# Kernel tuning notes

Measured on AMD Instinct MI355X. Metric: run time of the kernel, lower is better.

## Reference

```python
import jax, jax.numpy as jnp
import numpy as np

RATES = (6, 12, 18, 24)  # dilation/padding per branch


def _offset_conv(x, w, b, rate):
    # mmcv ConvModule with norm_cfg=None: conv (bias=True) + ReLU
    y = jax.lax.conv_general_dilated(
        x, w, window_strides=(1, 1),
        padding=[(rate, rate), (rate, rate)],
        rhs_dilation=(rate, rate),
        dimension_numbers=('NCHW', 'OIHW', 'NCHW'))
    return jax.nn.relu(y + b[None, :, None, None])


def _deform_conv(x, offset, w, rate):
    # DCNv1: 3x3 deformable conv, stride 1, padding=dilation=rate,
    # deformable_groups=1, no bias. Zero padding outside image (bilinear).
    B, C, H, W = x.shape
    K = 9  # 3x3 kernel taps, row-major; offset channels [2k]=dy, [2k+1]=dx
    ky = (jnp.arange(K) // 3 - 1).astype(x.dtype)
    kx = (jnp.arange(K) % 3 - 1).astype(x.dtype)
    off = offset.reshape(B, K, 2, H, W)
    gy = jnp.arange(H, dtype=x.dtype)
    gx = jnp.arange(W, dtype=x.dtype)
    # sampling coords [B,K,H,W]: p0 + dilated kernel offset + learned offset
    py = gy[None, None, :, None] + ky[None, :, None, None] * rate + off[:, :, 0]
    px = gx[None, None, None, :] + kx[None, :, None, None] * rate + off[:, :, 1]
    y0 = jnp.floor(py)
    x0 = jnp.floor(px)
    wy = (py - y0)[:, None]  # [B,1,K,H,W]
    wx = (px - x0)[:, None]
    y0i = y0.astype(jnp.int32)
    x0i = x0.astype(jnp.int32)
    xf = x.reshape(B, C, H * W)

    def gather(yi, xi):
        valid = (yi >= 0) & (yi < H) & (xi >= 0) & (xi < W)
        idx = (jnp.clip(yi, 0, H - 1) * W + jnp.clip(xi, 0, W - 1)).reshape(B, K * H * W)
        v = jnp.take_along_axis(xf, idx[:, None, :], axis=2).reshape(B, C, K, H, W)
        return v * valid[:, None].astype(x.dtype)

    samp = (gather(y0i, x0i) * (1 - wy) * (1 - wx)
            + gather(y0i, x0i + 1) * (1 - wy) * wx
            + gather(y0i + 1, x0i) * wy * (1 - wx)
            + gather(y0i + 1, x0i + 1) * wy * wx)  # [B,C,K,H,W]
    return jnp.einsum('oik,bikhw->bohw', w.reshape(w.shape[0], C, K), samp)


def setup_inputs() -> dict:
    key = jax.random.key(0)
    k1, k2, k3 = jax.random.split(key, 3)
    B, C, H, W = 2, 256, 64, 64
    Cout, R = 256, len(RATES)
    x = jax.random.normal(k1, (B, C, H, W), dtype=jnp.float32)
    dweights = jax.random.normal(k2, (R, Cout, C, 3, 3), dtype=jnp.float32) * 0.02
    oweights = jax.random.normal(k3, (R, 18, C, 3, 3), dtype=jnp.float32) * 0.01
    obias = jnp.zeros((R, 18), dtype=jnp.float32)
    return {"x": x, "dweights": dweights, "oweights": oweights, "obias": obias}


def reference(x, dweights, oweights, obias):
    R = len(RATES)
    outs = []
    for i in range(R):
        j = (i - 1) % R  # source quirk: offsets[i-1] (wraps to last for i=0)
        off = _offset_conv(x, oweights[j], obias[j], RATES[j])
        outs.append(_deform_conv(x, off, dweights[i], RATES[i]))
    return jnp.concatenate(outs, axis=1)
```

## Files before the change

kernel.cpp:

```cpp
#include <hip/hip_runtime.h>
#include <hip/hip_bf16.h>

typedef __attribute__((ext_vector_type(4))) float f32x4;
typedef __attribute__((ext_vector_type(2))) _Float16 h2;
typedef __attribute__((ext_vector_type(8))) _Float16 f16x8;

#define LGKM_BARRIER() asm volatile("s_waitcnt lgkmcnt(0)\n\ts_barrier" ::: "memory")

__device__ __forceinline__ uint4 lerp4(uint4 c0, uint4 c1, uint4 c2, uint4 c3,
                                       h2 qx, h2 qy, h2 qz, h2 qv) {
    h2 r0 = (*(h2*)&c0.x) * qx + (*(h2*)&c1.x) * qy + (*(h2*)&c2.x) * qz + (*(h2*)&c3.x) * qv;
    h2 r1 = (*(h2*)&c0.y) * qx + (*(h2*)&c1.y) * qy + (*(h2*)&c2.y) * qz + (*(h2*)&c3.y) * qv;
    h2 r2 = (*(h2*)&c0.z) * qx + (*(h2*)&c1.z) * qy + (*(h2*)&c2.z) * qz + (*(h2*)&c3.z) * qv;
    h2 r3 = (*(h2*)&c0.w) * qx + (*(h2*)&c1.w) * qy + (*(h2*)&c2.w) * qz + (*(h2*)&c3.w) * qv;
    return make_uint4(*(unsigned*)&r0, *(unsigned*)&r1, *(unsigned*)&r2, *(unsigned*)&r3);
}

__global__ __launch_bounds__(256) void transpose_x_hwc_f16(const float* __restrict__ x,
                                                           unsigned short* __restrict__ x16h) {
    __shared__ float s[64][65];
    int blk = blockIdx.x;
    int b = blk >> 8, ct = (blk >> 6) & 3, pt = blk & 63;
    int c0 = ct * 64, p0 = pt * 64;
    int tid = threadIdx.x;
    int tr = tid >> 6, tc = tid & 63;
#pragma unroll
    for (int i = 0; i < 16; ++i) {
        int c = i * 4 + tr;
        s[c][tc] = x[((size_t)b * 256 + c0 + c) * 4096 + p0 + tc];
    }
    __syncthreads();
#pragma unroll
    for (int i = 0; i < 16; ++i) {
        int pp = i * 4 + tr;
        _Float16 h = (_Float16)s[tc][pp];
        x16h[((size_t)b * 4096 + p0 + pp) * 256 + c0 + tc] = *(unsigned short*)&h;
    }
}

__global__ __launch_bounds__(256) void transpose_dw_f16(const float* __restrict__ dw,
                                                        unsigned short* __restrict__ wTh) {
    __shared__ float s[2304];
    int blk = blockIdx.x;
    int i = blk >> 8, o = blk & 255;
    const float* src = dw + (size_t)(i * 256 + o) * 2304;
    int tid = threadIdx.x;
#pragma unroll
    for (int e = tid; e < 576; e += 256)
        *(float4*)&s[e * 4] = *(const float4*)&src[e * 4];
    __syncthreads();
#pragma unroll
    for (int k = 0; k < 9; ++k) {
        _Float16 h = (_Float16)s[tid * 9 + k];
        wTh[(((size_t)i * 9 + k) * 256 + o) * 256 + tid] = *(unsigned short*)&h;
    }
}

__global__ __launch_bounds__(256) void transpose_ow_f16(const float* __restrict__ ow,
                                                        unsigned short* __restrict__ owTh) {
    int idx = blockIdx.x * 256 + threadIdx.x;
    int c = idx & 255;
    int m = (idx >> 8) & 31;
    int rk = idx >> 13;
    int k = rk % 9, r = rk / 9;
    float v = (m < 18) ? ow[((r * 18 + m) * 256 + c) * 9 + k] : 0.f;
    _Float16 h = (_Float16)v;
    owTh[idx] = *(unsigned short*)&h;
}

__global__ __launch_bounds__(512) void offset_mfma3f(const unsigned short* __restrict__ x16h,
                                                     const unsigned short* __restrict__ owTh,
                                                     const float* __restrict__ obias,
                                                     float* __restrict__ off) {
    __shared__ short    s_a[8][32][8];
    __shared__ short    s_b[8][128][8];
    __shared__ int      s_pix[9][128];
    __shared__ unsigned s_msk[9][128];

    const int blk = blockIdx.x;
    const int r = (blk & 7) >> 1, b = blk & 1;
    const int px0 = (blk >> 3) << 7;
    const int rate = 6 * (r + 1);

    const int tid = threadIdx.x;
    const int lane = tid & 63;
    const int w = tid >> 6;
    const int kg = lane >> 4, lm = lane & 15;
    const int sg = tid >> 7, spx = tid & 127;
    const int mA = (tid & 127) >> 2, kgA = tid & 3;

    const unsigned short* xbh = x16h + (size_t)b * 1048576;
    const unsigned short* wrb = owTh + (size_t)r * 9 * 32 * 256;

    for (int e = tid; e < 1152; e += 512) {
        int k = e >> 7, pl = e & 127;
        int pg = px0 + pl;
        int yy = (pg >> 6) + (k / 3 - 1) * rate;
        int xx = (pg & 63) + (k % 3 - 1) * rate;
        bool v = ((unsigned)yy < 64u) && ((unsigned)xx < 64u);
        int cy = min(max(yy, 0), 63), cx = min(max(xx, 0), 63);
        s_pix[k][pl] = cy * 64 + cx;
        s_msk[k][pl] = v ? 0xFFFFFFFFu : 0u;
    }
    __syncthreads();

    f32x4 acc0 = (f32x4)(0.f), acc1 = (f32x4)(0.f);

    uint4 a_lo, a_hi, v_lo, v_hi;
    if (tid < 128) {
        a_lo = *(const uint4*)(wrb + (size_t)mA * 256 + kgA * 8);
        a_hi = *(const uint4*)(wrb + (size_t)mA * 256 + 32 + kgA * 8);
    }
    {
        int pix = s_pix[0][spx];
        v_lo = *(const uint4*)(xbh + (size_t)pix * 256 + sg * 8);
        v_hi = *(const uint4*)(xbh + (size_t)pix * 256 + 32 + sg * 8);
    }
    unsigned m = s_msk[0][spx];

    for (int t = 0; t < 36; ++t) {
        uint4 pkl = make_uint4(v_lo.x & m, v_lo.y & m, v_lo.z & m, v_lo.w & m);
        uint4 pkh = make_uint4(v_hi.x & m, v_hi.y & m, v_hi.z & m, v_hi.w & m);

        LGKM_BARRIER();
        if (tid < 128) {
            *(uint4*)&s_a[kgA][mA][0]     = a_lo;
            *(uint4*)&s_a[kgA + 4][mA][0] = a_hi;
        }
        *(uint4*)&s_b[sg][spx][0]     = pkl;
        *(uint4*)&s_b[sg + 4][spx][0] = pkh;
        LGKM_BARRIER();

        if (t < 35) {
            int tn = t + 1, tapn = tn >> 2, c0n = (tn & 3) << 6;
            if (tid < 128) {
                a_lo = *(const uint4*)(wrb + ((size_t)tapn * 32 + mA) * 256 + c0n + kgA * 8);
                a_hi = *(const uint4*)(wrb + ((size_t)tapn * 32 + mA) * 256 + c0n + 32 + kgA * 8);
            }
            int pix = s_pix[tapn][spx];
            m = s_msk[tapn][spx];
            v_lo = *(const uint4*)(xbh + (size_t)pix * 256 + c0n + sg * 8);
            v_hi = *(const uint4*)(xbh + (size_t)pix * 256 + c0n + 32 + sg * 8);
        }

#pragma unroll
        for (int kf = 0; kf < 2; ++kf) {
            int oct = kf * 4 + kg;
            f16x8 bf  = *(const f16x8*)&s_b[oct][w * 16 + lm][0];
            f16x8 af0 = *(const f16x8*)&s_a[oct][lm][0];
            f16x8 af1 = *(const f16x8*)&s_a[oct][16 + lm][0];
            acc0 = __builtin_amdgcn_mfma_f32_16x16x32_f16(af0, bf, acc0, 0, 0, 0);
            acc1 = __builtin_amdgcn_mfma_f32_16x16x32_f16(af1, bf, acc1, 0, 0, 0);
        }
    }

    const float* bias = obias + r * 18;
    float* ob = off + (size_t)(r * 2 + b) * 18 * 4096;
    int px = px0 + w * 16 + lm;
#pragma unroll
    for (int reg = 0; reg < 4; ++reg) {
        int mm = kg * 4 + reg;
        ob[(size_t)mm * 4096 + px] = fmaxf(acc0[reg] + bias[mm], 0.f);
        int m1 = 16 + mm;
        if (m1 < 18)
            ob[(size_t)m1 * 4096 + px] = fmaxf(acc1[reg] + bias[m1], 0.f);
    }
}

__global__ __launch_bounds__(512, 2) void deform_mfma14(const unsigned short* __restrict__ x16h,
                                                        const unsigned short* __restrict__ wTh,
                                                        const float* __restrict__ off,
                                                        float* __restrict__ out) {
    __shared__ short s_a[2][256][64];
    __shared__ short s_b[2][64][64];

    const int blk = blockIdx.x;
    const int i = (blk & 7) >> 1, b = blk & 1;
    const int px0 = (blk >> 3) << 6;
    const int r = (i + 3) & 3;
    const int rate = 6 * (i + 1);

    const int tid = threadIdx.x;
    const int lane = tid & 63;
    const int w = tid >> 6;
    const int wo = w >> 1, wp = w & 1;
    const int kg = lane >> 4, lm = lane & 15;
    const int pxS = tid >> 3, chgS = tid & 7;
    const int oA = tid >> 3, partA = tid & 7;
    const int colA = (partA ^ (oA & 7)) * 8;

    const unsigned short* xbh = x16h + (size_t)b * 1048576;
    const float* offb = off + (size_t)(r * 2 + b) * 18 * 4096;
    const unsigned short* wib = wTh + (size_t)i * 9 * 65536;

    const int pg = px0 + pxS;
    const int yy = pg >> 6, xc = pg & 63;

    auto coords = [&](int k, float dy, float dx, int4& P, float4& Q) {
        float py = (float)(yy + (k / 3 - 1) * rate) + dy;
        float pxf = (float)(xc + (k % 3 - 1) * rate) + dx;
        float fy = floorf(py), fx = floorf(pxf);
        int y0 = (int)fy, x0 = (int)fx;
        float wy = py - fy, wx = pxf - fx;
        float vy0 = ((unsigned)y0 < 64u) ? 1.f : 0.f;
        float vy1 = ((unsigned)(y0 + 1) < 64u) ? 1.f : 0.f;
        float vx0 = ((unsigned)x0 < 64u) ? 1.f : 0.f;
        float vx1 = ((unsigned)(x0 + 1) < 64u) ? 1.f : 0.f;
        int cy0 = min(max(y0, 0), 63), cy1 = min(max(y0 + 1, 0), 63);
        int cx0 = min(max(x0, 0), 63), cx1 = min(max(x0 + 1, 0), 63);
        P = make_int4(cy0 * 64 + cx0, cy0 * 64 + cx1, cy1 * 64 + cx0, cy1 * 64 + cx1);
        Q = make_float4(vy0 * vx0 * (1.f - wy) * (1.f - wx),
                        vy0 * vx1 * (1.f - wy) * wx,
                        vy1 * vx0 * wy * (1.f - wx),
                        vy1 * vx1 * wy * wx);
    };

    f32x4 acc[4][2];
#pragma unroll
    for (int mi = 0; mi < 4; ++mi) {
        acc[mi][0] = (f32x4)(0.f);
        acc[mi][1] = (f32x4)(0.f);
    }

    uint4 a0, a1, a2, a3, v0, v1, v2, v3;

    auto load_step = [&](int t, int4 P) {
        int tap = t >> 2, c0 = (t & 3) << 6;
        const unsigned short* wrow = wib + (size_t)tap * 65536 + c0 + partA * 8;
        a0 = *(const uint4*)(wrow + (size_t)(oA      ) * 256);
        a1 = *(const uint4*)(wrow + (size_t)(oA +  64) * 256);
        a2 = *(const uint4*)(wrow + (size_t)(oA + 128) * 256);
        a3 = *(const uint4*)(wrow + (size_t)(oA + 192) * 256);
        const unsigned short* xch = xbh + c0 + chgS * 8;
        v0 = *(const uint4*)(xch + ((size_t)P.x << 8));
        v1 = *(const uint4*)(xch + ((size_t)P.y << 8));
        v2 = *(const uint4*)(xch + ((size_t)P.z << 8));
        v3 = *(const uint4*)(xch + ((size_t)P.w << 8));
    };

    auto stage_step = [&](int buf, float4 Q) {
        h2 qx = (h2)((_Float16)Q.x), qy = (h2)((_Float16)Q.y);
        h2 qz = (h2)((_Float16)Q.z), qv = (h2)((_Float16)Q.w);
        uint4 pk = lerp4(v0, v1, v2, v3, qx, qy, qz, qv);
        *(uint4*)&s_a[buf][oA      ][colA] = a0;
        *(uint4*)&s_a[buf][oA +  64][colA] = a1;
        *(uint4*)&s_a[buf][oA + 128][colA] = a2;
        *(uint4*)&s_a[buf][oA + 192][colA] = a3;
        *(uint4*)&s_b[buf][pxS][(chgS ^ (pxS & 7)) * 8] = pk;
    };

    int4 P;  float4 Q;
    int4 Pn; float4 Qn;
    float dyn, dxn;
    {
        float dy0 = offb[pg];
        float dx0 = offb[4096 + pg];
        coords(0, dy0, dx0, P, Q);
    }
    load_step(0, P);
    stage_step(0, Q);
    load_step(1, P);
    LGKM_BARRIER();

    for (int tap = 0; tap < 9; ++tap) {
#pragma unroll
        for (int sub = 0; sub < 4; ++sub) {
            const int t = tap * 4 + sub;
            const int rb = t & 1;

            if (sub == 0 && tap < 8) {
                dyn = offb[(size_t)(2 * (tap + 1)) * 4096 + pg];
                dxn = offb[(size_t)(2 * (tap + 1) + 1) * 4096 + pg];
            }
            if (sub == 1 && tap < 8)
                coords(tap + 1, dyn, dxn, Pn, Qn);

            if (t < 35) stage_step(rb ^ 1, (sub == 3 && tap < 8) ? Qn : Q);
            if (t < 34) load_step(t + 2, (sub >= 2 && tap < 8) ? Pn : P);

#pragma unroll
            for (int kf = 0; kf < 2; ++kf) {
                int oct = kf * 4 + kg;
                int bcol = (oct ^ (lm & 7)) * 8;
                f16x8 bf0 = *(const f16x8*)&s_b[rb][wp * 32 + lm][bcol];
                f16x8 bf1 = *(const f16x8*)&s_b[rb][wp * 32 + 16 + lm][bcol];
#pragma unroll
                for (int mi = 0; mi < 4; ++mi) {
                    int o = wo * 64 + mi * 16 + lm;
                    int col = (oct ^ (o & 7)) * 8;
                    f16x8 af = *(const f16x8*)&s_a[rb][o][col];
                    acc[mi][0] = __builtin_amdgcn_mfma_f32_16x16x32_f16(af, bf0, acc[mi][0], 0, 0, 0);
                    acc[mi][1] = __builtin_amdgcn_mfma_f32_16x16x32_f16(af, bf1, acc[mi][1], 0, 0, 0);
                }
            }

            LGKM_BARRIER();

            if (sub == 3 && tap < 8) { P = Pn; Q = Qn; }
        }
    }

    float* ob = out + ((size_t)b * 1024 + i * 256) * 4096;
#pragma unroll
    for (int mi = 0; mi < 4; ++mi) {
        int o = wo * 64 + mi * 16 + kg * 4;
#pragma unroll
        for (int ni = 0; ni < 2; ++ni) {
            int pgo = px0 + wp * 32 + ni * 16 + lm;
#pragma unroll
            for (int reg = 0; reg < 4; ++reg)
                ob[(size_t)(o + reg) * 4096 + pgo] = acc[mi][ni][reg];
        }
    }
}

extern "C" void kernel_launch(void* const* d_in, const int* in_sizes, int n_in,
                              void* d_out, int out_size, void* d_ws, size_t ws_size,
                              hipStream_t stream) {
    const float* x  = (const float*)d_in[0];
    const float* dw = (const float*)d_in[1];
    const float* ow = (const float*)d_in[2];
    const float* ob = (const float*)d_in[3];
    float* out = (float*)d_out;

    float* ws  = (float*)d_ws;
    float* off = ws;
    unsigned short* wTh  = (unsigned short*)(ws + 589824);
    unsigned short* owTh = wTh + 2359296;
    unsigned short* x16h = (unsigned short*)(ws + 1916928);

    transpose_x_hwc_f16<<<512, 256, 0, stream>>>(x, x16h);
    transpose_dw_f16<<<1024, 256, 0, stream>>>(dw, wTh);
    transpose_ow_f16<<<1152, 256, 0, stream>>>(ow, owTh);
    offset_mfma3f<<<256, 512, 0, stream>>>(x16h, owTh, ob, off);
    deform_mfma14<<<512, 512, 0, stream>>>(x16h, wTh, off, out);
}
```

Measured before the change: 115.2 us.

## Preformat deform weights into MFMA fragment layout and load A operands from global to registers

```diff
diff --git a/kernel.cpp b/kernel.cpp
--- a/kernel.cpp
+++ b/kernel.cpp
@@ -38,8 +38,8 @@
     }
 }
 
-__global__ __launch_bounds__(256) void transpose_dw_f16(const float* __restrict__ dw,
-                                                        unsigned short* __restrict__ wTh) {
+__global__ __launch_bounds__(256) void transpose_dw_frag(const float* __restrict__ dw,
+                                                         unsigned short* __restrict__ wfrag) {
     __shared__ float s[2304];
     int blk = blockIdx.x;
     int i = blk >> 8, o = blk & 255;
@@ -49,10 +49,12 @@
     for (int e = tid; e < 576; e += 256)
         *(float4*)&s[e * 4] = *(const float4*)&src[e * 4];
     __syncthreads();
+    int oct = (tid >> 3) & 7, e = tid & 7, sub = tid >> 6;
 #pragma unroll
     for (int k = 0; k < 9; ++k) {
         _Float16 h = (_Float16)s[tid * 9 + k];
-        wTh[(((size_t)i * 9 + k) * 256 + o) * 256 + tid] = *(unsigned short*)&h;
+        int t = k * 4 + sub;
+        wfrag[(((size_t)i * 36 + t) * 8 + oct) * 2048 + o * 8 + e] = *(unsigned short*)&h;
     }
 }
 
@@ -167,11 +169,10 @@
     }
 }
 
-__global__ __launch_bounds__(512, 2) void deform_mfma14(const unsigned short* __restrict__ x16h,
-                                                        const unsigned short* __restrict__ wTh,
+__global__ __launch_bounds__(512, 2) void deform_mfma15(const unsigned short* __restrict__ x16h,
+                                                        const unsigned short* __restrict__ wfrag,
                                                         const float* __restrict__ off,
                                                         float* __restrict__ out) {
-    __shared__ short s_a[2][256][64];
     __shared__ short s_b[2][64][64];
 
     const int blk = blockIdx.x;
@@ -186,12 +187,12 @@
     const int wo = w >> 1, wp = w & 1;
     const int kg = lane >> 4, lm = lane & 15;
     const int pxS = tid >> 3, chgS = tid & 7;
-    const int oA = tid >> 3, partA = tid & 7;
-    const int colA = (partA ^ (oA & 7)) * 8;
 
     const unsigned short* xbh = x16h + (size_t)b * 1048576;
     const float* offb = off + (size_t)(r * 2 + b) * 18 * 4096;
-    const unsigned short* wib = wTh + (size_t)i * 9 * 65536;
+    const unsigned short* wfi = wfrag + (size_t)i * 36 * 16384;
+    const unsigned short* wlaneA = wfi + (size_t)(kg    ) * 2048 + (size_t)(wo * 64 + lm) * 8;
+    const unsigned short* wlaneB = wfi + (size_t)(kg + 4) * 2048 + (size_t)(wo * 64 + lm) * 8;
 
     const int pg = px0 + pxS;
     const int yy = pg >> 6, xc = pg & 63;
@@ -222,30 +223,33 @@
         acc[mi][1] = (f32x4)(0.f);
     }
 
-    uint4 a0, a1, a2, a3, v0, v1, v2, v3;
-
-    auto load_step = [&](int t, int4 P) {
-        int tap = t >> 2, c0 = (t & 3) << 6;
-        const unsigned short* wrow = wib + (size_t)tap * 65536 + c0 + partA * 8;
-        a0 = *(const uint4*)(wrow + (size_t)(oA      ) * 256);
-        a1 = *(const uint4*)(wrow + (size_t)(oA +  64) * 256);
-        a2 = *(const uint4*)(wrow + (size_t)(oA + 128) * 256);
-        a3 = *(const uint4*)(wrow + (size_t)(oA + 192) * 256);
+    uint4 aA0, aA1, aA2, aA3, aB0, aB1, aB2, aB3;
+    uint4 v0, v1, v2, v3;
+
+    auto load_corners = [&](int t, int4 P) {
+        int c0 = (t & 3) << 6;
         const unsigned short* xch = xbh + c0 + chgS * 8;
         v0 = *(const uint4*)(xch + ((size_t)P.x << 8));
         v1 = *(const uint4*)(xch + ((size_t)P.y << 8));
         v2 = *(const uint4*)(xch + ((size_t)P.z << 8));
         v3 = *(const uint4*)(xch + ((size_t)P.w << 8));
     };
-
-    auto stage_step = [&](int buf, float4 Q) {
+    auto load_A = [&](int t) {
+        const unsigned short* ba = wlaneA + (size_t)t * 16384;
+        aA0 = *(const uint4*)(ba);
+        aA1 = *(const uint4*)(ba + 128);
+        aA2 = *(const uint4*)(ba + 256);
+        aA3 = *(const uint4*)(ba + 384);
+        const unsigned short* bb = wlaneB + (size_t)t * 16384;
+        aB0 = *(const uint4*)(bb);
+        aB1 = *(const uint4*)(bb + 128);
+        aB2 = *(const uint4*)(bb + 256);
+        aB3 = *(const uint4*)(bb + 384);
+    };
+    auto stage_B = [&](int buf, float4 Q) {
         h2 qx = (h2)((_Float16)Q.x), qy = (h2)((_Float16)Q.y);
         h2 qz = (h2)((_Float16)Q.z), qv = (h2)((_Float16)Q.w);
         uint4 pk = lerp4(v0, v1, v2, v3, qx, qy, qz, qv);
-        *(uint4*)&s_a[buf][oA      ][colA] = a0;
-        *(uint4*)&s_a[buf][oA +  64][colA] = a1;
-        *(uint4*)&s_a[buf][oA + 128][colA] = a2;
-        *(uint4*)&s_a[buf][oA + 192][colA] = a3;
         *(uint4*)&s_b[buf][pxS][(chgS ^ (pxS & 7)) * 8] = pk;
     };
 
@@ -257,9 +261,10 @@
         float dx0 = offb[4096 + pg];
         coords(0, dy0, dx0, P, Q);
     }
-    load_step(0, P);
-    stage_step(0, Q);
-    load_step(1, P);
+    load_corners(0, P);
+    stage_B(0, Q);
+    load_corners(1, P);
+    load_A(0);
     LGKM_BARRIER();
 
     for (int tap = 0; tap < 9; ++tap) {
@@ -275,24 +280,35 @@
             if (sub == 1 && tap < 8)
                 coords(tap + 1, dyn, dxn, Pn, Qn);
 
-            if (t < 35) stage_step(rb ^ 1, (sub == 3 && tap < 8) ? Qn : Q);
-            if (t < 34) load_step(t + 2, (sub >= 2 && tap < 8) ? Pn : P);
-
-#pragma unroll
-            for (int kf = 0; kf < 2; ++kf) {
-                int oct = kf * 4 + kg;
-                int bcol = (oct ^ (lm & 7)) * 8;
-                f16x8 bf0 = *(const f16x8*)&s_b[rb][wp * 32 + lm][bcol];
-                f16x8 bf1 = *(const f16x8*)&s_b[rb][wp * 32 + 16 + lm][bcol];
-#pragma unroll
-                for (int mi = 0; mi < 4; ++mi) {
-                    int o = wo * 64 + mi * 16 + lm;
-                    int col = (oct ^ (o & 7)) * 8;
-                    f16x8 af = *(const f16x8*)&s_a[rb][o][col];
-                    acc[mi][0] = __builtin_amdgcn_mfma_f32_16x16x32_f16(af, bf0, acc[mi][0], 0, 0, 0);
-                    acc[mi][1] = __builtin_amdgcn_mfma_f32_16x16x32_f16(af, bf1, acc[mi][1], 0, 0, 0);
-                }
+            if (t < 35) stage_B(rb ^ 1, (sub == 3 && tap < 8) ? Qn : Q);
+            if (t < 34) load_corners(t + 2, (sub >= 2 && tap < 8) ? Pn : P);
+
+            {
+                int bc0 = (kg ^ (lm & 7)) * 8;
+                f16x8 b00 = *(const f16x8*)&s_b[rb][wp * 32 + lm][bc0];
+                f16x8 b01 = *(const f16x8*)&s_b[rb][wp * 32 + 16 + lm][bc0];
+                acc[0][0] = __builtin_amdgcn_mfma_f32_16x16x32_f16(*(const f16x8*)&aA0, b00, acc[0][0], 0, 0, 0);
+                acc[0][1] = __builtin_amdgcn_mfma_f32_16x16x32_f16(*(const f16x8*)&aA0, b01, acc[0][1], 0, 0, 0);
+                acc[1][0] = __builtin_amdgcn_mfma_f32_16x16x32_f16(*(const f16x8*)&aA1, b00, acc[1][0], 0, 0, 0);
+                acc[1][1] = __builtin_amdgcn_mfma_f32_16x16x32_f16(*(const f16x8*)&aA1, b01, acc[1][1], 0, 0, 0);
+                acc[2][0] = __builtin_amdgcn_mfma_f32_16x16x32_f16(*(const f16x8*)&aA2, b00, acc[2][0], 0, 0, 0);
+                acc[2][1] = __builtin_amdgcn_mfma_f32_16x16x32_f16(*(const f16x8*)&aA2, b01, acc[2][1], 0, 0, 0);
+                acc[3][0] = __builtin_amdgcn_mfma_f32_16x16x32_f16(*(const f16x8*)&aA3, b00, acc[3][0], 0, 0, 0);
+                acc[3][1] = __builtin_amdgcn_mfma_f32_16x16x32_f16(*(const f16x8*)&aA3, b01, acc[3][1], 0, 0, 0);
+                int bc1 = ((kg + 4) ^ (lm & 7)) * 8;
+                f16x8 b10 = *(const f16x8*)&s_b[rb][wp * 32 + lm][bc1];
+                f16x8 b11 = *(const f16x8*)&s_b[rb][wp * 32 + 16 + lm][bc1];
+                acc[0][0] = __builtin_amdgcn_mfma_f32_16x16x32_f16(*(const f16x8*)&aB0, b10, acc[0][0], 0, 0, 0);
+                acc[0][1] = __builtin_amdgcn_mfma_f32_16x16x32_f16(*(const f16x8*)&aB0, b11, acc[0][1], 0, 0, 0);
+                acc[1][0] = __builtin_amdgcn_mfma_f32_16x16x32_f16(*(const f16x8*)&aB1, b10, acc[1][0], 0, 0, 0);
+                acc[1][1] = __builtin_amdgcn_mfma_f32_16x16x32_f16(*(const f16x8*)&aB1, b11, acc[1][1], 0, 0, 0);
+                acc[2][0] = __builtin_amdgcn_mfma_f32_16x16x32_f16(*(const f16x8*)&aB2, b10, acc[2][0], 0, 0, 0);
+                acc[2][1] = __builtin_amdgcn_mfma_f32_16x16x32_f16(*(const f16x8*)&aB2, b11, acc[2][1], 0, 0, 0);
+                acc[3][0] = __builtin_amdgcn_mfma_f32_16x16x32_f16(*(const f16x8*)&aB3, b10, acc[3][0], 0, 0, 0);
+                acc[3][1] = __builtin_amdgcn_mfma_f32_16x16x32_f16(*(const f16x8*)&aB3, b11, acc[3][1], 0, 0, 0);
             }
+
+            if (t < 35) load_A(t + 1);
 
             LGKM_BARRIER();
 
@@ -325,13 +341,13 @@
 
     float* ws  = (float*)d_ws;
     float* off = ws;
-    unsigned short* wTh  = (unsigned short*)(ws + 589824);
-    unsigned short* owTh = wTh + 2359296;
-    unsigned short* x16h = (unsigned short*)(ws + 1916928);
+    unsigned short* wfrag = (unsigned short*)(ws + 589824);
+    unsigned short* owTh  = wfrag + 2359296;
+    unsigned short* x16h  = (unsigned short*)(ws + 1916928);
 
     transpose_x_hwc_f16<<<512, 256, 0, stream>>>(x, x16h);
-    transpose_dw_f16<<<1024, 256, 0, stream>>>(dw, wTh);
+    transpose_dw_frag<<<1024, 256, 0, stream>>>(dw, wfrag);
     transpose_ow_f16<<<1152, 256, 0, stream>>>(ow, owTh);
     offset_mfma3f<<<256, 512, 0, stream>>>(x16h, owTh, ob, off);
-    deform_mfma14<<<512, 512, 0, stream>>>(x16h, wTh, off, out);
-}
+    deform_mfma15<<<512, 512, 0, stream>>>(x16h, wfrag, off, out);
+}
```

Result: no change. 116.8 us (+1.4%).

## Split deform conv output channels across blocks and single-buffer LDS staging

Applied to the files above, without the earlier changes.

```diff
diff --git a/kernel.cpp b/kernel.cpp
--- a/kernel.cpp
+++ b/kernel.cpp
@@ -167,16 +167,18 @@
     }
 }
 
-__global__ __launch_bounds__(512, 2) void deform_mfma14(const unsigned short* __restrict__ x16h,
+__global__ __launch_bounds__(256, 4) void deform_mfma16(const unsigned short* __restrict__ x16h,
                                                         const unsigned short* __restrict__ wTh,
                                                         const float* __restrict__ off,
                                                         float* __restrict__ out) {
-    __shared__ short s_a[2][256][64];
-    __shared__ short s_b[2][64][64];
+    __shared__ short s_a[128][64];
+    __shared__ short s_b[64][64];
 
     const int blk = blockIdx.x;
     const int i = (blk & 7) >> 1, b = blk & 1;
-    const int px0 = (blk >> 3) << 6;
+    const int oh = (blk >> 3) & 1;
+    const int px0 = (blk >> 4) << 6;
+    const int obase = oh << 7;
     const int r = (i + 3) & 3;
     const int rate = 6 * (i + 1);
 
@@ -185,9 +187,12 @@
     const int w = tid >> 6;
     const int wo = w >> 1, wp = w & 1;
     const int kg = lane >> 4, lm = lane & 15;
-    const int pxS = tid >> 3, chgS = tid & 7;
-    const int oA = tid >> 3, partA = tid & 7;
-    const int colA = (partA ^ (oA & 7)) * 8;
+    const int pxS = tid >> 2, cg = tid & 3;
+    const int oA = tid >> 1, pA = tid & 1;
+    const int c1A = ((pA * 4 + 0) ^ (oA & 7)) * 8;
+    const int c2A = ((pA * 4 + 1) ^ (oA & 7)) * 8;
+    const int c3A = ((pA * 4 + 2) ^ (oA & 7)) * 8;
+    const int c4A = ((pA * 4 + 3) ^ (oA & 7)) * 8;
 
     const unsigned short* xbh = x16h + (size_t)b * 1048576;
     const float* offb = off + (size_t)(r * 2 + b) * 18 * 4096;
@@ -222,31 +227,25 @@
         acc[mi][1] = (f32x4)(0.f);
     }
 
-    uint4 a0, a1, a2, a3, v0, v1, v2, v3;
+    uint4 a0, a1, a2, a3;
+    uint4 u0, u1, u2, u3, w0c, w1c, w2c, w3c;
 
     auto load_step = [&](int t, int4 P) {
         int tap = t >> 2, c0 = (t & 3) << 6;
-        const unsigned short* wrow = wib + (size_t)tap * 65536 + c0 + partA * 8;
-        a0 = *(const uint4*)(wrow + (size_t)(oA      ) * 256);
-        a1 = *(const uint4*)(wrow + (size_t)(oA +  64) * 256);
-        a2 = *(const uint4*)(wrow + (size_t)(oA + 128) * 256);
-        a3 = *(const uint4*)(wrow + (size_t)(oA + 192) * 256);
-        const unsigned short* xch = xbh + c0 + chgS * 8;
-        v0 = *(const uint4*)(xch + ((size_t)P.x << 8));
-        v1 = *(const uint4*)(xch + ((size_t)P.y << 8));
-        v2 = *(const uint4*)(xch + ((size_t)P.z << 8));
-        v3 = *(const uint4*)(xch + ((size_t)P.w << 8));
-    };
-
-    auto stage_step = [&](int buf, float4 Q) {
-        h2 qx = (h2)((_Float16)Q.x), qy = (h2)((_Float16)Q.y);
-        h2 qz = (h2)((_Float16)Q.z), qv = (h2)((_Float16)Q.w);
-        uint4 pk = lerp4(v0, v1, v2, v3, qx, qy, qz, qv);
-        *(uint4*)&s_a[buf][oA      ][colA] = a0;
-        *(uint4*)&s_a[buf][oA +  64][colA] = a1;
-        *(uint4*)&s_a[buf][oA + 128][colA] = a2;
-        *(uint4*)&s_a[buf][oA + 192][colA] = a3;
-        *(uint4*)&s_b[buf][pxS][(chgS ^ (pxS & 7)) * 8] = pk;
+        const unsigned short* wrow = wib + ((size_t)tap * 256 + obase + oA) * 256 + c0 + pA * 32;
+        a0 = *(const uint4*)(wrow);
+        a1 = *(const uint4*)(wrow + 8);
+        a2 = *(const uint4*)(wrow + 16);
+        a3 = *(const uint4*)(wrow + 24);
+        const unsigned short* xch = xbh + c0 + cg * 8;
+        u0 = *(const uint4*)(xch + ((size_t)P.x << 8));
+        u1 = *(const uint4*)(xch + ((size_t)P.y << 8));
+        u2 = *(const uint4*)(xch + ((size_t)P.z << 8));
+        u3 = *(const uint4*)(xch + ((size_t)P.w << 8));
+        w0c = *(const uint4*)(xch + ((size_t)P.x << 8) + 32);
+        w1c = *(const uint4*)(xch + ((size_t)P.y << 8) + 32);
+        w2c = *(const uint4*)(xch + ((size_t)P.z << 8) + 32);
+        w3c = *(const uint4*)(xch + ((size_t)P.w << 8) + 32);
     };
 
     int4 P;  float4 Q;
@@ -258,15 +257,11 @@
         coords(0, dy0, dx0, P, Q);
     }
     load_step(0, P);
-    stage_step(0, Q);
-    load_step(1, P);
-    LGKM_BARRIER();
 
     for (int tap = 0; tap < 9; ++tap) {
 #pragma unroll
         for (int sub = 0; sub < 4; ++sub) {
             const int t = tap * 4 + sub;
-            const int rb = t & 1;
 
             if (sub == 0 && tap < 8) {
                 dyn = offb[(size_t)(2 * (tap + 1)) * 4096 + pg];
@@ -275,32 +270,47 @@
             if (sub == 1 && tap < 8)
                 coords(tap + 1, dyn, dxn, Pn, Qn);
 
-            if (t < 35) stage_step(rb ^ 1, (sub == 3 && tap < 8) ? Qn : Q);
-            if (t < 34) load_step(t + 2, (sub >= 2 && tap < 8) ? Pn : P);
+            uint4 pkA, pkB;
+            {
+                h2 qx = (h2)((_Float16)Q.x), qy = (h2)((_Float16)Q.y);
+                h2 qz = (h2)((_Float16)Q.z), qv = (h2)((_Float16)Q.w);
+                pkA = lerp4(u0, u1, u2, u3, qx, qy, qz, qv);
+                pkB = lerp4(w0c, w1c, w2c, w3c, qx, qy, qz, qv);
+            }
+
+            LGKM_BARRIER();
+            *(uint4*)&s_a[oA][c1A] = a0;
+            *(uint4*)&s_a[oA][c2A] = a1;
+            *(uint4*)&s_a[oA][c3A] = a2;
+            *(uint4*)&s_a[oA][c4A] = a3;
+            *(uint4*)&s_b[pxS][(cg ^ (pxS & 7)) * 8]       = pkA;
+            *(uint4*)&s_b[pxS][((cg + 4) ^ (pxS & 7)) * 8] = pkB;
+            LGKM_BARRIER();
+
+            if (t < 35)
+                load_step(t + 1, (sub == 3 && tap < 8) ? Pn : P);
 
 #pragma unroll
             for (int kf = 0; kf < 2; ++kf) {
                 int oct = kf * 4 + kg;
                 int bcol = (oct ^ (lm & 7)) * 8;
-                f16x8 bf0 = *(const f16x8*)&s_b[rb][wp * 32 + lm][bcol];
-                f16x8 bf1 = *(const f16x8*)&s_b[rb][wp * 32 + 16 + lm][bcol];
+                f16x8 bf0 = *(const f16x8*)&s_b[wp * 32 + lm][bcol];
+                f16x8 bf1 = *(const f16x8*)&s_b[wp * 32 + 16 + lm][bcol];
 #pragma unroll
                 for (int mi = 0; mi < 4; ++mi) {
                     int o = wo * 64 + mi * 16 + lm;
                     int col = (oct ^ (o & 7)) * 8;
-                    f16x8 af = *(const f16x8*)&s_a[rb][o][col];
+                    f16x8 af = *(const f16x8*)&s_a[o][col];
                     acc[mi][0] = __builtin_amdgcn_mfma_f32_16x16x32_f16(af, bf0, acc[mi][0], 0, 0, 0);
                     acc[mi][1] = __builtin_amdgcn_mfma_f32_16x16x32_f16(af, bf1, acc[mi][1], 0, 0, 0);
                 }
             }
 
-            LGKM_BARRIER();
-
             if (sub == 3 && tap < 8) { P = Pn; Q = Qn; }
         }
     }
 
-    float* ob = out + ((size_t)b * 1024 + i * 256) * 4096;
+    float* ob = out + ((size_t)b * 1024 + i * 256 + obase) * 4096;
 #pragma unroll
     for (int mi = 0; mi < 4; ++mi) {
         int o = wo * 64 + mi * 16 + kg * 4;
@@ -333,5 +343,5 @@
     transpose_dw_f16<<<1024, 256, 0, stream>>>(dw, wTh);
     transpose_ow_f16<<<1152, 256, 0, stream>>>(ow, owTh);
     offset_mfma3f<<<256, 512, 0, stream>>>(x16h, owTh, ob, off);
-    deform_mfma14<<<512, 512, 0, stream>>>(x16h, wTh, off, out);
-}
+    deform_mfma16<<<1024, 256, 0, stream>>>(x16h, wTh, off, out);
+}
```

Measured after the change: 128.3 us. +11.4%, slower.

## Replace double-buffered LDS pipeline in deform kernel with single buffer and two barriers

Applied to the files above, without the earlier changes.

```diff
diff --git a/kernel.cpp b/kernel.cpp
--- a/kernel.cpp
+++ b/kernel.cpp
@@ -167,12 +167,12 @@
     }
 }
 
-__global__ __launch_bounds__(512, 2) void deform_mfma14(const unsigned short* __restrict__ x16h,
+__global__ __launch_bounds__(512, 2) void deform_mfma17(const unsigned short* __restrict__ x16h,
                                                         const unsigned short* __restrict__ wTh,
                                                         const float* __restrict__ off,
                                                         float* __restrict__ out) {
-    __shared__ short s_a[2][256][64];
-    __shared__ short s_b[2][64][64];
+    __shared__ short s_a[256][64];
+    __shared__ short s_b[64][64];
 
     const int blk = blockIdx.x;
     const int i = (blk & 7) >> 1, b = blk & 1;
@@ -238,17 +238,6 @@
         v3 = *(const uint4*)(xch + ((size_t)P.w << 8));
     };
 
-    auto stage_step = [&](int buf, float4 Q) {
-        h2 qx = (h2)((_Float16)Q.x), qy = (h2)((_Float16)Q.y);
-        h2 qz = (h2)((_Float16)Q.z), qv = (h2)((_Float16)Q.w);
-        uint4 pk = lerp4(v0, v1, v2, v3, qx, qy, qz, qv);
-        *(uint4*)&s_a[buf][oA      ][colA] = a0;
-        *(uint4*)&s_a[buf][oA +  64][colA] = a1;
-        *(uint4*)&s_a[buf][oA + 128][colA] = a2;
-        *(uint4*)&s_a[buf][oA + 192][colA] = a3;
-        *(uint4*)&s_b[buf][pxS][(chgS ^ (pxS & 7)) * 8] = pk;
-    };
-
     int4 P;  float4 Q;
     int4 Pn; float4 Qn;
     float dyn, dxn;
@@ -258,15 +247,11 @@
         coords(0, dy0, dx0, P, Q);
     }
     load_step(0, P);
-    stage_step(0, Q);
-    load_step(1, P);
-    LGKM_BARRIER();
 
     for (int tap = 0; tap < 9; ++tap) {
 #pragma unroll
         for (int sub = 0; sub < 4; ++sub) {
             const int t = tap * 4 + sub;
-            const int rb = t & 1;
 
             if (sub == 0 && tap < 8) {
                 dyn = offb[(size_t)(2 * (tap + 1)) * 4096 + pg];
@@ -275,26 +260,39 @@
             if (sub == 1 && tap < 8)
                 coords(tap + 1, dyn, dxn, Pn, Qn);
 
-            if (t < 35) stage_step(rb ^ 1, (sub == 3 && tap < 8) ? Qn : Q);
-            if (t < 34) load_step(t + 2, (sub >= 2 && tap < 8) ? Pn : P);
+            uint4 pk;
+            {
+                h2 qx = (h2)((_Float16)Q.x), qy = (h2)((_Float16)Q.y);
+                h2 qz = (h2)((_Float16)Q.z), qv = (h2)((_Float16)Q.w);
+                pk = lerp4(v0, v1, v2, v3, qx, qy, qz, qv);
+            }
+
+            LGKM_BARRIER();
+            *(uint4*)&s_a[oA      ][colA] = a0;
+            *(uint4*)&s_a[oA +  64][colA] = a1;
+            *(uint4*)&s_a[oA + 128][colA] = a2;
+            *(uint4*)&s_a[oA + 192][colA] = a3;
+            *(uint4*)&s_b[pxS][(chgS ^ (pxS & 7)) * 8] = pk;
+            LGKM_BARRIER();
+
+            if (t < 35)
+                load_step(t + 1, (sub == 3 && tap < 8) ? Pn : P);
 
 #pragma unroll
             for (int kf = 0; kf < 2; ++kf) {
                 int oct = kf * 4 + kg;
                 int bcol = (oct ^ (lm & 7)) * 8;
-                f16x8 bf0 = *(const f16x8*)&s_b[rb][wp * 32 + lm][bcol];
-                f16x8 bf1 = *(const f16x8*)&s_b[rb][wp * 32 + 16 + lm][bcol];
+                f16x8 bf0 = *(const f16x8*)&s_b[wp * 32 + lm][bcol];
+                f16x8 bf1 = *(const f16x8*)&s_b[wp * 32 + 16 + lm][bcol];
 #pragma unroll
                 for (int mi = 0; mi < 4; ++mi) {
                     int o = wo * 64 + mi * 16 + lm;
                     int col = (oct ^ (o & 7)) * 8;
-                    f16x8 af = *(const f16x8*)&s_a[rb][o][col];
+                    f16x8 af = *(const f16x8*)&s_a[o][col];
                     acc[mi][0] = __builtin_amdgcn_mfma_f32_16x16x32_f16(af, bf0, acc[mi][0], 0, 0, 0);
                     acc[mi][1] = __builtin_amdgcn_mfma_f32_16x16x32_f16(af, bf1, acc[mi][1], 0, 0, 0);
                 }
             }
-
-            LGKM_BARRIER();
 
             if (sub == 3 && tap < 8) { P = Pn; Q = Qn; }
         }
@@ -333,5 +331,5 @@
     transpose_dw_f16<<<1024, 256, 0, stream>>>(dw, wTh);
     transpose_ow_f16<<<1152, 256, 0, stream>>>(ow, owTh);
     offset_mfma3f<<<256, 512, 0, stream>>>(x16h, owTh, ob, off);
-    deform_mfma14<<<512, 512, 0, stream>>>(x16h, wTh, off, out);
-}
+    deform_mfma17<<<512, 512, 0, stream>>>(x16h, wTh, off, out);
+}
```

Result: slower. 129.2 us (+12.2%).
